# Optimization experiments

Measured on AMD Instinct MI355X. Metric: run time of the kernel, lower is better.

## Reference

```python
import jax, jax.numpy as jnp
import numpy as np

E, K, NG, TG = 64, 8, 8, 4   # num_experts, top_k, num_expert_group, topk_group
CAP = 1024
SCALE = 2.5                   # routed_scaling_factor


def setup_inputs() -> dict:
    key = jax.random.key(0)
    ks = jax.random.split(key, 9)
    B, S, H, F = 1, 2048, 1024, 512
    bound = 1.0 / 32.0  # kaiming_uniform(a=sqrt(5)) on [E, H]: sqrt(6/(6*H))
    return {
        "hidden_states": jax.random.normal(ks[0], (B, S, H), jnp.float32),
        "gate_weight": jax.random.uniform(ks[1], (E, H), jnp.float32, -bound, bound),
        "e_bias": jnp.zeros((E,), jnp.float32),
        "w1": jax.random.normal(ks[2], (E, F, H), jnp.float32) * 0.02,
        "w2": jax.random.normal(ks[3], (E, H, F), jnp.float32) * 0.02,
        "w3": jax.random.normal(ks[4], (E, F, H), jnp.float32) * 0.02,
        "shared_gate": jax.random.normal(ks[5], (2 * F, H), jnp.float32) * 0.02,
        "shared_up": jax.random.normal(ks[6], (2 * F, H), jnp.float32) * 0.02,
        "shared_down": jax.random.normal(ks[7], (H, 2 * F), jnp.float32) * 0.02,
    }


def _route(x_flat, gate_weight, e_bias):
    T = x_flat.shape[0]
    logits = x_flat.astype(jnp.float32) @ gate_weight.astype(jnp.float32).T  # [T,E]
    scores = jax.nn.sigmoid(logits)
    sfc = scores + e_bias[None, :]
    # group-limited routing: keep TG of NG groups by sum of top-2 scores per group
    group_scores = jax.lax.top_k(sfc.reshape(T, NG, E // NG), 2)[0].sum(-1)  # [T,NG]
    _, gidx = jax.lax.top_k(group_scores, TG)
    gmask = jnp.zeros((T, NG), jnp.float32).at[jnp.arange(T)[:, None], gidx].set(1.0)
    smask = jnp.repeat(gmask, E // NG, axis=1)  # [T,E]
    tmp = jnp.where(smask > 0, sfc, 0.0)
    _, topk_idx = jax.lax.top_k(tmp, K)  # [T,K]
    topk_w = jnp.take_along_axis(scores, topk_idx, axis=1)
    topk_w = topk_w / (topk_w.sum(-1, keepdims=True) + 1e-20)
    return topk_idx, topk_w * SCALE


def _moe_forward(hidden_states, gate_weight, e_bias, w1, w2, w3,
                 shared_gate, shared_up, shared_down):
    B, S, H = hidden_states.shape
    T = B * S
    x = hidden_states.reshape(T, H)
    topk_idx, topk_w = _route(x, gate_weight, e_bias)

    # --- dispatch: sort slots by expert, compute position within expert ---
    Sk = T * K
    flat_e = topk_idx.reshape(-1)                      # [Sk]
    order = jnp.argsort(flat_e)                        # stable sort
    sorted_e = flat_e[order]
    counts = jax.ops.segment_sum(jnp.ones((Sk,), jnp.int32), flat_e, num_segments=E)
    offsets = jnp.cumsum(counts) - counts              # exclusive prefix
    pos = jnp.arange(Sk) - offsets[sorted_e]           # position within expert
    tok_sorted = x[order // K]                         # [Sk,H]

    xe = jnp.zeros((E, CAP, H), x.dtype).at[sorted_e, pos].set(tok_sorted, mode="drop")
    # --- grouped SwiGLU expert MLP ---
    h = jax.nn.silu(jnp.einsum("ech,efh->ecf", xe, w1)) * jnp.einsum("ech,efh->ecf", xe, w3)
    ye = jnp.einsum("ecf,ehf->ech", h, w2)             # [E,CAP,H]

    # --- combine: gather back, weight, scatter-add per token ---
    pos_c = jnp.minimum(pos, CAP - 1)
    vals = ye[sorted_e, pos_c]
    vals = jnp.where((pos < CAP)[:, None], vals, 0.0)
    flat_w = topk_w.reshape(-1)[order].astype(vals.dtype)
    flat_t = (jnp.arange(Sk) // K)[order]
    out = jax.ops.segment_sum(vals * flat_w[:, None], flat_t, num_segments=T)

    # --- shared expert (SwiGLU MLP over all tokens) ---
    shared = (jax.nn.silu(x @ shared_gate.T) * (x @ shared_up.T)) @ shared_down.T
    return (out + shared).reshape(B, S, H)


def reference(hidden_states, gate_weight, e_bias, w1, w2, w3,
              shared_gate, shared_up, shared_down):
    return _moe_forward(hidden_states, gate_weight, e_bias, w1, w2, w3,
                        shared_gate, shared_up, shared_down)
```

## Files before the change

### kernel.cpp

```cpp
#include <hip/hip_runtime.h>

#define T_TOK 2048
#define HDIM  1024
#define FDIM  512
#define NEXP  64
#define TOPK  8
#define NGRP  8
#define TGRP  4
#define CAPC  1024
#define SCALE_F 2.5f

typedef _Float16 f16;
typedef _Float16 f16x4 __attribute__((ext_vector_type(4)));
typedef _Float16 f16x8 __attribute__((ext_vector_type(8)));
typedef float    f32x4 __attribute__((ext_vector_type(4)));

typedef const __attribute__((address_space(1))) void* gas_t;
typedef __attribute__((address_space(3))) void* las_t;
__device__ __forceinline__ void gl2lds16(const void* g, void* l) {
    __builtin_amdgcn_global_load_lds((gas_t)g, (las_t)l, 16, 0, 0);
}
#define FRAG(S, r, s) (*(const f16x8*)&S[(r)*64 + (((s) ^ ((r)&7)))*8])

__global__ void k_cvt(const float* __restrict__ src, f16* __restrict__ dst, int n8)
{
    int i = blockIdx.x * blockDim.x + threadIdx.x;
    if (i >= n8) return;
    const float4* s = (const float4*)src + (size_t)i * 2;
    float4 a = s[0], b = s[1];
    f16x8 h = { (f16)a.x, (f16)a.y, (f16)a.z, (f16)a.w,
                (f16)b.x, (f16)b.y, (f16)b.z, (f16)b.w };
    *(f16x8*)(dst + (size_t)i * 8) = h;
}

__global__ void k_route(const float* __restrict__ x, const float* __restrict__ gw,
                        const float* __restrict__ ebias,
                        f16* __restrict__ xb,
                        int* __restrict__ counts,
                        int* __restrict__ slot_e, int* __restrict__ slot_pos,
                        float* __restrict__ slot_w)
{
    int t = blockIdx.x;
    int lane = threadIdx.x;
    __shared__ float4 sx[HDIM / 4];
    __shared__ float sS[NEXP], sF[NEXP];
    __shared__ float gsc[NGRP];
    __shared__ unsigned gmask_s;
    __shared__ int sIdx[TOPK];

    const float4* xr = (const float4*)(x + (size_t)t * HDIM);
    for (int i = lane; i < HDIM / 4; i += 64) sx[i] = xr[i];
    __syncthreads();

    for (int i = lane; i < HDIM / 4; i += 64) {
        float4 v = sx[i];
        f16x4 h = { (f16)v.x, (f16)v.y, (f16)v.z, (f16)v.w };
        *(f16x4*)(xb + (size_t)t * HDIM + i * 4) = h;
    }

    const float4* wr = (const float4*)(gw + (size_t)lane * HDIM);
    float acc = 0.f;
    #pragma unroll 8
    for (int i = 0; i < HDIM / 4; ++i) {
        float4 a = sx[i]; float4 b = wr[i];
        acc += a.x * b.x + a.y * b.y + a.z * b.z + a.w * b.w;
    }
    float score = 1.f / (1.f + __expf(-acc));
    float sfc = score + ebias[lane];
    sS[lane] = score; sF[lane] = sfc;
    __syncthreads();

    if (lane < NGRP) {
        float m1 = -1e30f, m2 = -1e30f;
        for (int j = 0; j < NEXP / NGRP; ++j) {
            float v = sF[lane * (NEXP / NGRP) + j];
            if (v > m1) { m2 = m1; m1 = v; } else if (v > m2) m2 = v;
        }
        gsc[lane] = m1 + m2;
    }
    __syncthreads();
    if (lane == 0) {
        unsigned gm = 0;
        for (int s = 0; s < TGRP; ++s) {
            float best = -1e30f; int bg = 0;
            for (int g = 0; g < NGRP; ++g)
                if (!((gm >> g) & 1) && gsc[g] > best) { best = gsc[g]; bg = g; }
            gm |= 1u << bg;
        }
        gmask_s = gm;
    }
    __syncthreads();

    float vv = ((gmask_s >> (lane >> 3)) & 1) ? sfc : 0.0f;
    for (int k = 0; k < TOPK; ++k) {
        float bv = vv; int bi = lane;
        for (int off = 32; off; off >>= 1) {
            float ov = __shfl_down(bv, off);
            int   oi = __shfl_down(bi, off);
            if (ov > bv || (ov == bv && oi < bi)) { bv = ov; bi = oi; }
        }
        bi = __shfl(bi, 0);
        if (lane == bi) vv = -1e30f;
        if (lane == 0) sIdx[k] = bi;
    }
    __syncthreads();
    if (lane == 0) {
        float sum = 0.f;
        for (int k = 0; k < TOPK; ++k) sum += sS[sIdx[k]];
        float inv = SCALE_F / (sum + 1e-20f);
        for (int k = 0; k < TOPK; ++k) {
            int e = sIdx[k];
            int pos = atomicAdd(&counts[e], 1);
            int s = t * TOPK + k;
            slot_e[s] = e; slot_pos[s] = pos; slot_w[s] = sS[e] * inv;
        }
    }
}

__global__ void k_scan(const int* __restrict__ counts, int* __restrict__ offsets)
{
    if (threadIdx.x == 0) {
        int s = 0;
        for (int e = 0; e < NEXP; ++e) { offsets[e] = s; s += counts[e]; }
    }
}

__global__ void k_rowmap(const int* __restrict__ slot_e, const int* __restrict__ slot_pos,
                         const int* __restrict__ offsets, int* __restrict__ row_tok)
{
    int s = blockIdx.x * 256 + threadIdx.x;
    if (s >= T_TOK * TOPK) return;
    int p = slot_pos[s];
    if (p >= CAPC) return;
    row_tok[offsets[slot_e[s]] + p] = s >> 3;
}

__global__ __launch_bounds__(256, 2) void k_gateup(
    const f16* __restrict__ A, const f16* __restrict__ W1,
    const f16* __restrict__ W3, f16* __restrict__ Hout,
    const int* __restrict__ offsets, const int* __restrict__ counts,
    const int* __restrict__ row_tok,
    int K, int Nld, int Mtot, int expert_mode)
{
    int e = expert_mode ? blockIdx.z : 0;
    int rowbeg = expert_mode ? offsets[e] : 0;
    int M = expert_mode ? (counts[e] < CAPC ? counts[e] : CAPC) : Mtot;
    int mtile = blockIdx.y * 128;
    if (mtile >= M) return;
    int Mblk = M - mtile; if (Mblk > 128) Mblk = 128;
    int n0 = blockIdx.x * 64;
    const f16* W1e = W1 + (size_t)e * Nld * K;
    const f16* W3e = W3 + (size_t)e * Nld * K;

    __shared__ __align__(16) f16 sA[128 * 64];
    __shared__ __align__(16) f16 sB1[64 * 64];
    __shared__ __align__(16) f16 sB3[64 * 64];

    int tid = threadIdx.x, wave = tid >> 6, lane = tid & 63;
    int subrow = lane >> 3;
    int lseg = (lane & 7) ^ subrow;

    const f16* aptr[4];
    #pragma unroll
    for (int c = 0; c < 4; ++c) {
        int r = (wave * 4 + c) * 8 + subrow;
        int rr = (r < Mblk) ? r : 0;
        size_t srow = expert_mode ? (size_t)row_tok[rowbeg + mtile + rr]
                                  : (size_t)(rowbeg + mtile + rr);
        aptr[c] = A + srow * (size_t)K + lseg * 8;
    }
    const f16 *b1ptr[2], *b3ptr[2];
    #pragma unroll
    for (int c = 0; c < 2; ++c) {
        int r = (wave * 2 + c) * 8 + subrow;
        b1ptr[c] = W1e + (size_t)(n0 + r) * K + lseg * 8;
        b3ptr[c] = W3e + (size_t)(n0 + r) * K + lseg * 8;
    }

    int lrow = lane & 15, lquad = lane >> 4;
    int wm = (wave & 1) * 64, wn = (wave >> 1) * 32;

    f32x4 accg[4][2], accu[4][2];
    #pragma unroll
    for (int i = 0; i < 4; ++i)
        #pragma unroll
        for (int j = 0; j < 2; ++j) {
            f32x4 z = {0.f, 0.f, 0.f, 0.f};
            accg[i][j] = z; accu[i][j] = z;
        }

    for (int k0 = 0; k0 < K; k0 += 64) {
        #pragma unroll
        for (int c = 0; c < 4; ++c)
            gl2lds16(aptr[c] + k0, &sA[(wave * 4 + c) * 512]);
        #pragma unroll
        for (int c = 0; c < 2; ++c) {
            gl2lds16(b1ptr[c] + k0, &sB1[(wave * 2 + c) * 512]);
            gl2lds16(b3ptr[c] + k0, &sB3[(wave * 2 + c) * 512]);
        }
        __syncthreads();
        #pragma unroll
        for (int ks = 0; ks < 2; ++ks) {
            int seg = ks * 4 + lquad;
            f16x8 a[4], b1[2], b3[2];
            #pragma unroll
            for (int i = 0; i < 4; ++i) a[i] = FRAG(sA, wm + i * 16 + lrow, seg);
            #pragma unroll
            for (int j = 0; j < 2; ++j) {
                b1[j] = FRAG(sB1, wn + j * 16 + lrow, seg);
                b3[j] = FRAG(sB3, wn + j * 16 + lrow, seg);
            }
            #pragma unroll
            for (int i = 0; i < 4; ++i)
                #pragma unroll
                for (int j = 0; j < 2; ++j) {
                    accg[i][j] = __builtin_amdgcn_mfma_f32_16x16x32_f16(a[i], b1[j], accg[i][j], 0, 0, 0);
                    accu[i][j] = __builtin_amdgcn_mfma_f32_16x16x32_f16(a[i], b3[j], accu[i][j], 0, 0, 0);
                }
        }
        __syncthreads();
    }

    f16* Hrow = Hout + (size_t)(rowbeg + mtile) * Nld + n0;
    #pragma unroll
    for (int i = 0; i < 4; ++i)
        #pragma unroll
        for (int j = 0; j < 2; ++j)
            #pragma unroll
            for (int r = 0; r < 4; ++r) {
                int m = wm + i * 16 + lquad * 4 + r;
                if (m < Mblk) {
                    int n = wn + j * 16 + lrow;
                    float g = accg[i][j][r], u = accu[i][j][r];
                    float h = g / (1.f + __expf(-g)) * u;
                    Hrow[(size_t)m * Nld + n] = (f16)h;
                }
            }
}

__global__ __launch_bounds__(256, 2) void k_down(
    const f16* __restrict__ A, const f16* __restrict__ W,
    f16* __restrict__ Y,
    const int* __restrict__ offsets, const int* __restrict__ counts,
    int K, int Nld, int Mtot, int expert_mode)
{
    int e = expert_mode ? blockIdx.z : 0;
    int rowbeg = expert_mode ? offsets[e] : 0;
    int M = expert_mode ? (counts[e] < CAPC ? counts[e] : CAPC) : Mtot;
    int mtile = blockIdx.y * 128;
    if (mtile >= M) return;
    int Mblk = M - mtile; if (Mblk > 128) Mblk = 128;
    int n0 = blockIdx.x * 128;
    const f16* We = W + (size_t)e * Nld * K;

    __shared__ __align__(16) f16 sA[128 * 64];
    __shared__ __align__(16) f16 sW[128 * 64];

    int tid = threadIdx.x, wave = tid >> 6, lane = tid & 63;
    int subrow = lane >> 3;
    int lseg = (lane & 7) ^ subrow;

    const f16 *aptr[4], *wptr[4];
    #pragma unroll
    for (int c = 0; c < 4; ++c) {
        int r = (wave * 4 + c) * 8 + subrow;
        int rr = (r < Mblk) ? r : 0;
        aptr[c] = A + (size_t)(rowbeg + mtile + rr) * K + lseg * 8;
        wptr[c] = We + (size_t)(n0 + r) * K + lseg * 8;
    }

    int lrow = lane & 15, lquad = lane >> 4;
    int wm = (wave & 1) * 64, wn = (wave >> 1) * 64;

    f32x4 acc[4][4];
    #pragma unroll
    for (int i = 0; i < 4; ++i)
        #pragma unroll
        for (int j = 0; j < 4; ++j) { f32x4 z = {0.f, 0.f, 0.f, 0.f}; acc[i][j] = z; }

    for (int k0 = 0; k0 < K; k0 += 64) {
        #pragma unroll
        for (int c = 0; c < 4; ++c) {
            gl2lds16(aptr[c] + k0, &sA[(wave * 4 + c) * 512]);
            gl2lds16(wptr[c] + k0, &sW[(wave * 4 + c) * 512]);
        }
        __syncthreads();
        #pragma unroll
        for (int ks = 0; ks < 2; ++ks) {
            int seg = ks * 4 + lquad;
            f16x8 a[4], b[4];
            #pragma unroll
            for (int i = 0; i < 4; ++i) a[i] = FRAG(sA, wm + i * 16 + lrow, seg);
            #pragma unroll
            for (int j = 0; j < 4; ++j) b[j] = FRAG(sW, wn + j * 16 + lrow, seg);
            #pragma unroll
            for (int i = 0; i < 4; ++i)
                #pragma unroll
                for (int j = 0; j < 4; ++j)
                    acc[i][j] = __builtin_amdgcn_mfma_f32_16x16x32_f16(a[i], b[j], acc[i][j], 0, 0, 0);
        }
        __syncthreads();
    }

    f16* Yrow = Y + (size_t)(rowbeg + mtile) * Nld + n0;
    #pragma unroll
    for (int i = 0; i < 4; ++i)
        #pragma unroll
        for (int j = 0; j < 4; ++j)
            #pragma unroll
            for (int r = 0; r < 4; ++r) {
                int m = wm + i * 16 + lquad * 4 + r;
                if (m < Mblk)
                    Yrow[(size_t)m * Nld + wn + j * 16 + lrow] = (f16)acc[i][j][r];
            }
}

__global__ void k_combine(const f16* __restrict__ y, const f16* __restrict__ ys,
                          const int* __restrict__ slot_e, const int* __restrict__ slot_pos,
                          const float* __restrict__ slot_w, const int* __restrict__ offsets,
                          float* __restrict__ out)
{
    int t = blockIdx.x, i = threadIdx.x;
    size_t col = (size_t)i * 4;
    f16x4 s = *(const f16x4*)(ys + (size_t)t * HDIM + col);
    float a0 = (float)s[0], a1 = (float)s[1], a2 = (float)s[2], a3 = (float)s[3];
    #pragma unroll
    for (int k = 0; k < TOPK; ++k) {
        int sidx = t * TOPK + k;
        int p = slot_pos[sidx];
        if (p < CAPC) {
            int row = offsets[slot_e[sidx]] + p;
            float w = slot_w[sidx];
            f16x4 v = *(const f16x4*)(y + (size_t)row * HDIM + col);
            a0 += w * (float)v[0]; a1 += w * (float)v[1];
            a2 += w * (float)v[2]; a3 += w * (float)v[3];
        }
    }
    float4 o = {a0, a1, a2, a3};
    *(float4*)(out + (size_t)t * HDIM + col) = o;
}

extern "C" void kernel_launch(void* const* d_in, const int* in_sizes, int n_in,
                              void* d_out, int out_size, void* d_ws, size_t ws_size,
                              hipStream_t stream)
{
    const float* x  = (const float*)d_in[0];
    const float* gw = (const float*)d_in[1];
    const float* eb = (const float*)d_in[2];
    const float* w1 = (const float*)d_in[3];
    const float* w2 = (const float*)d_in[4];
    const float* w3 = (const float*)d_in[5];
    const float* sg = (const float*)d_in[6];
    const float* su = (const float*)d_in[7];
    const float* sd = (const float*)d_in[8];
    float* out = (float*)d_out;

    char* p = (char*)d_ws;
    size_t off = 0;
    auto alloc = [&](size_t n) { void* r = p + off; off = (off + n + 255) & ~(size_t)255; return r; };
    int*   counts   = (int*)alloc(NEXP * 4);
    int*   offsets  = (int*)alloc(NEXP * 4);
    int*   slot_e   = (int*)alloc((size_t)T_TOK * TOPK * 4);
    int*   slot_pos = (int*)alloc((size_t)T_TOK * TOPK * 4);
    float* slot_w   = (float*)alloc((size_t)T_TOK * TOPK * 4);
    int*   row_tok  = (int*)alloc((size_t)T_TOK * TOPK * 4);
    f16*   xb  = (f16*)alloc((size_t)T_TOK * HDIM * 2);
    f16*   h   = (f16*)alloc((size_t)T_TOK * TOPK * FDIM * 2);
    f16*   y   = (f16*)alloc((size_t)T_TOK * TOPK * HDIM * 2);
    f16*   hs  = (f16*)alloc((size_t)T_TOK * 2 * FDIM * 2);
    f16*   ys  = (f16*)alloc((size_t)T_TOK * HDIM * 2);
    f16*   wbufA = (f16*)alloc((size_t)NEXP * FDIM * HDIM * 2);
    f16*   wbufB = (f16*)alloc((size_t)NEXP * FDIM * HDIM * 2);
    f16*   sgh = (f16*)alloc((size_t)2 * FDIM * HDIM * 2);
    f16*   suh = (f16*)alloc((size_t)2 * FDIM * HDIM * 2);
    f16*   sdh = (f16*)alloc((size_t)HDIM * 2 * FDIM * 2);

    hipMemsetAsync(counts, 0, NEXP * 4, stream);
    k_route<<<T_TOK, 64, 0, stream>>>(x, gw, eb, xb, counts, slot_e, slot_pos, slot_w);
    k_scan<<<1, 64, 0, stream>>>(counts, offsets);
    k_rowmap<<<(T_TOK * TOPK + 255) / 256, 256, 0, stream>>>(slot_e, slot_pos, offsets, row_tok);

    const int EW8 = NEXP * FDIM * HDIM / 8;
    const int SW8 = 2 * FDIM * HDIM / 8;
    k_cvt<<<(EW8 + 255) / 256, 256, 0, stream>>>(w1, wbufA, EW8);
    k_cvt<<<(EW8 + 255) / 256, 256, 0, stream>>>(w3, wbufB, EW8);
    k_cvt<<<(SW8 + 255) / 256, 256, 0, stream>>>(sg, sgh, SW8);
    k_cvt<<<(SW8 + 255) / 256, 256, 0, stream>>>(su, suh, SW8);
    k_cvt<<<(SW8 + 255) / 256, 256, 0, stream>>>(sd, sdh, SW8);

    k_gateup<<<dim3(FDIM / 64, CAPC / 128, NEXP), 256, 0, stream>>>(
        xb, wbufA, wbufB, h, offsets, counts, row_tok, HDIM, FDIM, 0, 1);
    k_gateup<<<dim3((2 * FDIM) / 64, T_TOK / 128, 1), 256, 0, stream>>>(
        xb, sgh, suh, hs, offsets, counts, row_tok, HDIM, 2 * FDIM, T_TOK, 0);

    k_cvt<<<(EW8 + 255) / 256, 256, 0, stream>>>(w2, wbufA, EW8);

    k_down<<<dim3(HDIM / 128, CAPC / 128, NEXP), 256, 0, stream>>>(
        h, wbufA, y, offsets, counts, FDIM, HDIM, 0, 1);
    k_down<<<dim3(HDIM / 128, T_TOK / 128, 1), 256, 0, stream>>>(
        hs, sdh, ys, offsets, counts, 2 * FDIM, HDIM, T_TOK, 0);

    k_combine<<<T_TOK, 256, 0, stream>>>(y, ys, slot_e, slot_pos, slot_w, offsets, out);
}
```

Baseline: 730.3 us.

## Split routing into tiled logits GEMM and separate top-k kernel

The per-token routing kernel, which had each lane stream a full gate-weight row from global memory, is split in three. An x-to-f16 conversion now runs through the generic convert kernel. A tiled logits kernel stages 8 tokens and all 64 gate rows in LDS, so gate weights are reused across tokens. A lightweight top-k kernel then reads the precomputed logits. This cuts redundant gate-weight global traffic at the cost of two extra launches and a logits buffer round trip.

```diff
diff --git a/kernel.cpp b/kernel.cpp
--- a/kernel.cpp
+++ b/kernel.cpp
@@ -33,39 +33,63 @@
     *(f16x8*)(dst + (size_t)i * 8) = h;
 }
 
-__global__ void k_route(const float* __restrict__ x, const float* __restrict__ gw,
-                        const float* __restrict__ ebias,
-                        f16* __restrict__ xb,
-                        int* __restrict__ counts,
-                        int* __restrict__ slot_e, int* __restrict__ slot_pos,
-                        float* __restrict__ slot_w)
+__global__ __launch_bounds__(256) void k_logits(const float* __restrict__ x,
+                                                const float* __restrict__ gw,
+                                                float* __restrict__ logits)
+{
+    __shared__ float sX[8][132];
+    __shared__ float sGW[64][132];
+    int tid = threadIdx.x;
+    int t0 = blockIdx.x * 8;
+    int tl = tid & 7;
+    int eb = tid >> 3;
+    f32x4 acc0 = {0.f,0.f,0.f,0.f}, acc1 = {0.f,0.f,0.f,0.f};
+
+    for (int hc0 = 0; hc0 < HDIM; hc0 += 128) {
+        __syncthreads();
+        {
+            int row = tid >> 5, c4 = tid & 31;
+            float4 v = *(const float4*)(x + (size_t)(t0 + row) * HDIM + hc0 + c4 * 4);
+            *(float4*)&sX[row][c4 * 4] = v;
+        }
+        #pragma unroll
+        for (int k = 0; k < 8; ++k) {
+            int row = k * 8 + (tid >> 5), c4 = tid & 31;
+            float4 v = *(const float4*)(gw + (size_t)row * HDIM + hc0 + c4 * 4);
+            *(float4*)&sGW[row][c4 * 4] = v;
+        }
+        __syncthreads();
+        #pragma unroll
+        for (int c4 = 0; c4 < 32; ++c4) {
+            float4 ax = *(const float4*)&sX[tl][c4 * 4];
+            float4 g0 = *(const float4*)&sGW[eb][c4 * 4];
+            float4 g1 = *(const float4*)&sGW[eb + 32][c4 * 4];
+            acc0.x += ax.x * g0.x; acc0.y += ax.y * g0.y;
+            acc0.z += ax.z * g0.z; acc0.w += ax.w * g0.w;
+            acc1.x += ax.x * g1.x; acc1.y += ax.y * g1.y;
+            acc1.z += ax.z * g1.z; acc1.w += ax.w * g1.w;
+        }
+    }
+    float l0 = (acc0.x + acc0.y) + (acc0.z + acc0.w);
+    float l1 = (acc1.x + acc1.y) + (acc1.z + acc1.w);
+    logits[(size_t)(t0 + tl) * NEXP + eb]      = l0;
+    logits[(size_t)(t0 + tl) * NEXP + eb + 32] = l1;
+}
+
+__global__ void k_topk(const float* __restrict__ logits, const float* __restrict__ ebias,
+                       int* __restrict__ counts,
+                       int* __restrict__ slot_e, int* __restrict__ slot_pos,
+                       float* __restrict__ slot_w)
 {
     int t = blockIdx.x;
     int lane = threadIdx.x;
-    __shared__ float4 sx[HDIM / 4];
     __shared__ float sS[NEXP], sF[NEXP];
     __shared__ float gsc[NGRP];
     __shared__ unsigned gmask_s;
     __shared__ int sIdx[TOPK];
 
-    const float4* xr = (const float4*)(x + (size_t)t * HDIM);
-    for (int i = lane; i < HDIM / 4; i += 64) sx[i] = xr[i];
-    __syncthreads();
-
-    for (int i = lane; i < HDIM / 4; i += 64) {
-        float4 v = sx[i];
-        f16x4 h = { (f16)v.x, (f16)v.y, (f16)v.z, (f16)v.w };
-        *(f16x4*)(xb + (size_t)t * HDIM + i * 4) = h;
-    }
-
-    const float4* wr = (const float4*)(gw + (size_t)lane * HDIM);
-    float acc = 0.f;
-    #pragma unroll 8
-    for (int i = 0; i < HDIM / 4; ++i) {
-        float4 a = sx[i]; float4 b = wr[i];
-        acc += a.x * b.x + a.y * b.y + a.z * b.z + a.w * b.w;
-    }
-    float score = 1.f / (1.f + __expf(-acc));
+    float logit = logits[(size_t)t * NEXP + lane];
+    float score = 1.f / (1.f + __expf(-logit));
     float sfc = score + ebias[lane];
     sS[lane] = score; sF[lane] = sfc;
     __syncthreads();
@@ -364,6 +388,7 @@
     int*   slot_pos = (int*)alloc((size_t)T_TOK * TOPK * 4);
     float* slot_w   = (float*)alloc((size_t)T_TOK * TOPK * 4);
     int*   row_tok  = (int*)alloc((size_t)T_TOK * TOPK * 4);
+    float* logits   = (float*)alloc((size_t)T_TOK * NEXP * 4);
     f16*   xb  = (f16*)alloc((size_t)T_TOK * HDIM * 2);
     f16*   h   = (f16*)alloc((size_t)T_TOK * TOPK * FDIM * 2);
     f16*   y   = (f16*)alloc((size_t)T_TOK * TOPK * HDIM * 2);
@@ -376,7 +401,11 @@
     f16*   sdh = (f16*)alloc((size_t)HDIM * 2 * FDIM * 2);
 
     hipMemsetAsync(counts, 0, NEXP * 4, stream);
-    k_route<<<T_TOK, 64, 0, stream>>>(x, gw, eb, xb, counts, slot_e, slot_pos, slot_w);
+
+    const int XW8 = T_TOK * HDIM / 8;
+    k_cvt<<<(XW8 + 255) / 256, 256, 0, stream>>>(x, xb, XW8);
+    k_logits<<<T_TOK / 8, 256, 0, stream>>>(x, gw, logits);
+    k_topk<<<T_TOK, 64, 0, stream>>>(logits, eb, counts, slot_e, slot_pos, slot_w);
     k_scan<<<1, 64, 0, stream>>>(counts, offsets);
     k_rowmap<<<(T_TOK * TOPK + 255) / 256, 256, 0, stream>>>(slot_e, slot_pos, offsets, row_tok);
 
```

Measured after the change: 692.4 us. -5.2%, faster.
